# Performance work log

Measured on AMD Instinct MI355X. Metric: run time of the kernel, lower is better.

Reference implementation:

```python
import jax, jax.numpy as jnp
import numpy as np

B, N, D = 4, 4096, 128
LOSS_WEIGHT = 1.0  # module hardcodes self.loss_weight = 1.0


def setup_inputs() -> dict:
    key = jax.random.key(0)
    k1, k2 = jax.random.split(key)
    corr_pred = jax.random.normal(k1, (B, N, D), dtype=jnp.float32)
    corr_target = jax.random.normal(k2, (B, N, D), dtype=jnp.float32)
    return {"corr_pred": corr_pred, "corr_target": corr_target}


def chamfer_distance(x, y):
    # x: [B, N, D], y: [B, N, D]
    x2 = jnp.sum(x * x, axis=-1)                      # [B, N]  diag of x @ x^T
    y2 = jnp.sum(y * y, axis=-1)                      # [B, N]  diag of y @ y^T
    zz = jnp.einsum('bnd,bmd->bnm', x, y)             # [B, N, N]
    # P[b,i,j] = ||x_i||^2 + ||y_j||^2 - 2 x_i . y_j
    P = x2[:, :, None] + y2[:, None, :] - 2.0 * zz
    P = jnp.clip(P, 0.0, 100.0)
    return jnp.mean(jnp.min(P, axis=1)) + jnp.mean(jnp.min(P, axis=2))


def reference(corr_pred, corr_target):
    chamfer = chamfer_distance(corr_pred, corr_target)
    return LOSS_WEIGHT * chamfer / corr_target.shape[0]
```

## Files before the change

kernel.cpp:

```cpp
#include <hip/hip_runtime.h>
#include <hip/hip_bf16.h>

#define B_ 4
#define N_ 4096
#define D_ 128
#define EPB (N_ * D_)
#define COFF 1024.0f

typedef float f32x4 __attribute__((ext_vector_type(4)));
typedef int   int8v __attribute__((ext_vector_type(8)));
typedef int   int4v __attribute__((ext_vector_type(4)));

#define SQRT2 1.41421356237309515f


__global__ __launch_bounds__(256) void prep_kernel(
    const float* __restrict__ X, const float* __restrict__ Y,
    unsigned char* __restrict__ Xb, unsigned char* __restrict__ Yb,
    float* __restrict__ x2, float* __restrict__ y2,
    int* __restrict__ rowmin, int* __restrict__ colmin)
{
    const int which = blockIdx.y;
    const float* __restrict__ src = which ? Y : X;
    unsigned char* __restrict__ dst = which ? Yb : Xb;
    float* __restrict__ nrm = which ? y2 : x2;
    int* __restrict__ mn = which ? colmin : rowmin;

    const int t = threadIdx.x;
    const int r = t >> 4, c = t & 15;
    const int rgG = blockIdx.x;
    const int row = rgG * 16 + r;

    const float4 v0 = *(const float4*)(src + (size_t)row * D_ + c * 8);
    const float4 v1 = *(const float4*)(src + (size_t)row * D_ + c * 8 + 4);

    float sq = v0.x * v0.x;
    sq = fmaf(v0.y, v0.y, sq); sq = fmaf(v0.z, v0.z, sq); sq = fmaf(v0.w, v0.w, sq);
    sq = fmaf(v1.x, v1.x, sq); sq = fmaf(v1.y, v1.y, sq);
    sq = fmaf(v1.z, v1.z, sq); sq = fmaf(v1.w, v1.w, sq);
    #pragma unroll
    for (int m = 1; m < 16; m <<= 1) sq += __shfl_xor(sq, m);

    unsigned lo = 0, hi = 0;
    lo = __builtin_amdgcn_cvt_pk_fp8_f32(v0.x * SQRT2, v0.y * SQRT2, lo, false);
    lo = __builtin_amdgcn_cvt_pk_fp8_f32(v0.z * SQRT2, v0.w * SQRT2, lo, true);
    hi = __builtin_amdgcn_cvt_pk_fp8_f32(v1.x * SQRT2, v1.y * SQRT2, hi, false);
    hi = __builtin_amdgcn_cvt_pk_fp8_f32(v1.z * SQRT2, v1.w * SQRT2, hi, true);

    const int b = row >> 12;
    const int rg = (row & (N_ - 1)) >> 4;
    uint2 packed; packed.x = lo; packed.y = hi;
    *(uint2*)(dst + (size_t)b * EPB + rg * 2048 + (c >> 2) * 512
              + r * 32 + (c & 3) * 8) = packed;

    if (c == 0) {
        nrm[row] = sq;
        mn[row] = 0x7f7fffff;
    }
}


#define PREF(B0, B1, Y0, Y1, H) do {                                          \
    const int cb_ = jc * 256 + (H) * 32;                                      \
    const unsigned char* bp0_ = Yp + (size_t)(cb_ >> 4) * 2048                \
                               + quad * 512 + l16 * 32;                       \
    const int4v lo0_ = *(const int4v*)(bp0_);                                 \
    const int4v hi0_ = *(const int4v*)(bp0_ + 16);                            \
    const int4v lo1_ = *(const int4v*)(bp0_ + 2048);                          \
    const int4v hi1_ = *(const int4v*)(bp0_ + 2064);                          \
    B0 = (int8v){lo0_.x, lo0_.y, lo0_.z, lo0_.w, hi0_.x, hi0_.y, hi0_.z, hi0_.w}; \
    B1 = (int8v){lo1_.x, lo1_.y, lo1_.z, lo1_.w, hi1_.x, hi1_.y, hi1_.z, hi1_.w}; \
    Y0 = y2[(size_t)b * N_ + cb_ + l16];                                      \
    Y1 = y2[(size_t)b * N_ + cb_ + 16 + l16];                                 \
} while (0)

#define STEP(B0, B1, Y0, Y1, H) do {                                          \
    f32x4 acc0_[4], acc1_[4];                                                 \
    _Pragma("unroll")                                                         \
    for (int rt = 0; rt < 4; rt++) {                                          \
        acc0_[rt] = (f32x4){0.f, 0.f, 0.f, 0.f};                              \
        acc1_[rt] = (f32x4){0.f, 0.f, 0.f, 0.f};                              \
    }                                                                         \
    _Pragma("unroll")                                                         \
    for (int rt = 0; rt < 4; rt++) {                                          \
        acc0_[rt] = __builtin_amdgcn_mfma_scale_f32_16x16x128_f8f6f4(         \
            af[rt], B0, acc0_[rt], 0, 0, 0, 127, 0, 127);                     \
        acc1_[rt] = __builtin_amdgcn_mfma_scale_f32_16x16x128_f8f6f4(         \
            af[rt], B1, acc1_[rt], 0, 0, 0, 127, 0, 127);                     \
    }                                                                         \
    float cm0_ = 3.0e38f, cm1_ = 3.0e38f;                                     \
    _Pragma("unroll")                                                         \
    for (int rt = 0; rt < 4; rt++)                                            \
    _Pragma("unroll")                                                         \
    for (int i = 0; i < 4; i++) {                                             \
        const float xv_ = x2v[rt][i];                                         \
        const float a0_ = acc0_[rt][i], a1_ = acc1_[rt][i];                   \
        rmin[rt][i] = fminf(rmin[rt][i], fminf(Y0 - a0_, Y1 - a1_));          \
        cm0_ = fminf(cm0_, xv_ - a0_);                                        \
        cm1_ = fminf(cm1_, xv_ - a1_);                                        \
    }                                                                         \
    {                                                                         \
        const int cb_ = jc * 256 + (H) * 32;                                  \
        float v0_ = fminf(cm0_, __shfl_xor(cm0_, 16));                        \
        v0_ = fminf(v0_, __shfl_xor(v0_, 32));                                \
        float v1_ = fminf(cm1_, __shfl_xor(cm1_, 16));                        \
        v1_ = fminf(v1_, __shfl_xor(v1_, 32));                                \
        if (quad == 0) {                                                      \
            atomicMin(&colmin[(size_t)b * N_ + cb_ + l16],                    \
                      __float_as_int(v0_ + COFF));                            \
            atomicMin(&colmin[(size_t)b * N_ + cb_ + 16 + l16],               \
                      __float_as_int(v1_ + COFF));                            \
        }                                                                     \
    }                                                                         \
} while (0)

__global__ __launch_bounds__(256, 2) void chamfer_mfma(
    const unsigned char* __restrict__ Xb, const unsigned char* __restrict__ Yb,
    const float* __restrict__ x2, const float* __restrict__ y2,
    int* __restrict__ rowmin, int* __restrict__ colmin)
{
    const int b = blockIdx.z;
    const int iT = blockIdx.y;
    const int jc = blockIdx.x;
    const int tid = threadIdx.x;
    const int wave = tid >> 6, lane = tid & 63;
    const int quad = lane >> 4, l16 = lane & 15;
    const int rowBase = iT * 256 + wave * 64;

    const unsigned char* __restrict__ Xp = Xb + (size_t)b * EPB;
    const unsigned char* __restrict__ Yp = Yb + (size_t)b * EPB;

    int8v af[4];
    #pragma unroll
    for (int rt = 0; rt < 4; rt++) {
        const unsigned char* ap = Xp + ((rowBase >> 4) + rt) * 2048
                                 + quad * 512 + l16 * 32;
        const int4v lo = *(const int4v*)(ap);
        const int4v hi = *(const int4v*)(ap + 16);
        af[rt] = (int8v){lo.x, lo.y, lo.z, lo.w, hi.x, hi.y, hi.z, hi.w};
    }
    f32x4 x2v[4];
    #pragma unroll
    for (int rt = 0; rt < 4; rt++)
        x2v[rt] = *(const f32x4*)(x2 + (size_t)b * N_ + rowBase + rt * 16 + quad * 4);

    float rmin[4][4];
    #pragma unroll
    for (int rt = 0; rt < 4; rt++)
        #pragma unroll
        for (int i = 0; i < 4; i++) rmin[rt][i] = 3.0e38f;

    int8v bA0, bA1, bB0, bB1;
    float yA0, yA1, yB0, yB1;
    PREF(bA0, bA1, yA0, yA1, 0);

    #pragma clang loop unroll(disable)
    for (int sp = 0; sp < 4; ++sp) {
        const int h0 = sp * 2;
        PREF(bB0, bB1, yB0, yB1, h0 + 1);
        STEP(bA0, bA1, yA0, yA1, h0);
        if (sp < 3)
            PREF(bA0, bA1, yA0, yA1, h0 + 2);
        STEP(bB0, bB1, yB0, yB1, h0 + 1);
    }

    #pragma unroll
    for (int rt = 0; rt < 4; rt++)
        #pragma unroll
        for (int i = 0; i < 4; i++) {
            float v = rmin[rt][i];
            #pragma unroll
            for (int m = 1; m < 16; m <<= 1) v = fminf(v, __shfl_xor(v, m));
            if (l16 == 0) {
                float c = fminf(fmaxf(x2v[rt][i] + v, 0.0f), 100.0f);
                atomicMin(&rowmin[(size_t)b * N_ + rowBase + rt * 16 + quad * 4 + i],
                          __float_as_int(c));
            }
        }
}

__global__ __launch_bounds__(256) void finalize1_kernel(
    const int* __restrict__ rowmin, const int* __restrict__ colmin,
    const float* __restrict__ y2, float* __restrict__ partial)
{
    const int i = blockIdx.x * 256 + threadIdx.x;
    float s;
    {
        int4 v = ((const int4*)rowmin)[i];
        s  = __int_as_float(v.x) + __int_as_float(v.y) +
             __int_as_float(v.z) + __int_as_float(v.w);
        int4 c = ((const int4*)colmin)[i];
        float4 yv = ((const float4*)y2)[i];
        s += fminf(fmaxf(__int_as_float(c.x) - COFF + yv.x, 0.f), 100.f);
        s += fminf(fmaxf(__int_as_float(c.y) - COFF + yv.y, 0.f), 100.f);
        s += fminf(fmaxf(__int_as_float(c.z) - COFF + yv.z, 0.f), 100.f);
        s += fminf(fmaxf(__int_as_float(c.w) - COFF + yv.w, 0.f), 100.f);
    }
    #pragma unroll
    for (int m = 1; m < 64; m <<= 1) s += __shfl_xor(s, m);
    __shared__ float sm[4];
    if ((threadIdx.x & 63) == 0) sm[threadIdx.x >> 6] = s;
    __syncthreads();
    if (threadIdx.x == 0)
        partial[blockIdx.x] = sm[0] + sm[1] + sm[2] + sm[3];
}

__global__ __launch_bounds__(64) void finalize2_kernel(
    const float* __restrict__ partial, float* __restrict__ out)
{
    const int l = threadIdx.x;
    float s = (l < 16) ? partial[l] : 0.f;
    #pragma unroll
    for (int m = 1; m < 16; m <<= 1) s += __shfl_xor(s, m);
    if (l == 0)
        out[0] = s / ((float)B_ * (float)N_) / (float)B_;
}

extern "C" void kernel_launch(void* const* d_in, const int* in_sizes, int n_in,
                              void* d_out, int out_size, void* d_ws, size_t ws_size,
                              hipStream_t stream) {
    const float* X = (const float*)d_in[0];
    const float* Y = (const float*)d_in[1];

    char* ws = (char*)d_ws;
    const size_t f8_bytes = (size_t)B_ * N_ * D_;
    unsigned char* Xb = (unsigned char*)ws;
    unsigned char* Yb = (unsigned char*)(ws + f8_bytes);
    char* ws2 = ws + 2 * f8_bytes;
    const size_t vec_bytes = (size_t)B_ * N_ * 4;
    float* x2      = (float*)(ws2);
    float* y2      = (float*)(ws2 + vec_bytes);
    int*   rowmin  = (int*)  (ws2 + 2 * vec_bytes);
    int*   colmin  = (int*)  (ws2 + 3 * vec_bytes);
    float* partial = (float*)(ws2 + 4 * vec_bytes);
    float* out = (float*)d_out;

    prep_kernel<<<dim3(B_ * N_ / 16, 2), 256, 0, stream>>>(
        X, Y, Xb, Yb, x2, y2, rowmin, colmin);
    chamfer_mfma<<<dim3(16, N_ / 256, B_), 256, 0, stream>>>(
        Xb, Yb, x2, y2, rowmin, colmin);
    finalize1_kernel<<<16, 256, 0, stream>>>(rowmin, colmin, y2, partial);
    finalize2_kernel<<<1, 64, 0, stream>>>(partial, out);
}
```

Before: 91.38 us.

## Replace global atomicMin reductions with per-block partial buffers reduced in finalize

Row and column minima are no longer merged with global atomicMin. Instead, each block and wave writes its partial minima to dedicated slices of a workspace buffer, and finalize1 reduces over the 16 row partials and 64 column partials for each element. This removes atomic contention and the init stores in prep, at the cost of a much larger workspace (about 80 vectors) and more memory traffic in the finalize pass, which now runs on 64 blocks.

```diff
diff --git a/kernel.cpp b/kernel.cpp
--- a/kernel.cpp
+++ b/kernel.cpp
@@ -5,7 +5,6 @@
 #define N_ 4096
 #define D_ 128
 #define EPB (N_ * D_)
-#define COFF 1024.0f
 
 typedef float f32x4 __attribute__((ext_vector_type(4)));
 typedef int   int8v __attribute__((ext_vector_type(8)));
@@ -17,14 +16,12 @@
 __global__ __launch_bounds__(256) void prep_kernel(
     const float* __restrict__ X, const float* __restrict__ Y,
     unsigned char* __restrict__ Xb, unsigned char* __restrict__ Yb,
-    float* __restrict__ x2, float* __restrict__ y2,
-    int* __restrict__ rowmin, int* __restrict__ colmin)
+    float* __restrict__ x2, float* __restrict__ y2)
 {
     const int which = blockIdx.y;
     const float* __restrict__ src = which ? Y : X;
     unsigned char* __restrict__ dst = which ? Yb : Xb;
     float* __restrict__ nrm = which ? y2 : x2;
-    int* __restrict__ mn = which ? colmin : rowmin;
 
     const int t = threadIdx.x;
     const int r = t >> 4, c = t & 15;
@@ -53,10 +50,7 @@
     *(uint2*)(dst + (size_t)b * EPB + rg * 2048 + (c >> 2) * 512
               + r * 32 + (c & 3) * 8) = packed;
 
-    if (c == 0) {
-        nrm[row] = sq;
-        mn[row] = 0x7f7fffff;
-    }
+    if (c == 0) nrm[row] = sq;
 }
 
 
@@ -106,10 +100,8 @@
         float v1_ = fminf(cm1_, __shfl_xor(cm1_, 16));                        \
         v1_ = fminf(v1_, __shfl_xor(v1_, 32));                                \
         if (quad == 0) {                                                      \
-            atomicMin(&colmin[(size_t)b * N_ + cb_ + l16],                    \
-                      __float_as_int(v0_ + COFF));                            \
-            atomicMin(&colmin[(size_t)b * N_ + cb_ + 16 + l16],               \
-                      __float_as_int(v1_ + COFF));                            \
+            cpart[cpb + cb_ + l16] = v0_;                                     \
+            cpart[cpb + cb_ + 16 + l16] = v1_;                                \
         }                                                                     \
     }                                                                         \
 } while (0)
@@ -117,7 +109,7 @@
 __global__ __launch_bounds__(256, 2) void chamfer_mfma(
     const unsigned char* __restrict__ Xb, const unsigned char* __restrict__ Yb,
     const float* __restrict__ x2, const float* __restrict__ y2,
-    int* __restrict__ rowmin, int* __restrict__ colmin)
+    float* __restrict__ rpart, float* __restrict__ cpart)
 {
     const int b = blockIdx.z;
     const int iT = blockIdx.y;
@@ -126,6 +118,8 @@
     const int wave = tid >> 6, lane = tid & 63;
     const int quad = lane >> 4, l16 = lane & 15;
     const int rowBase = iT * 256 + wave * 64;
+    const size_t cpb = (size_t)((b * 16 + iT) * 4 + wave) * N_;
+    const size_t rpb = (size_t)(b * 16 + jc) * N_;
 
     const unsigned char* __restrict__ Xp = Xb + (size_t)b * EPB;
     const unsigned char* __restrict__ Yp = Yb + (size_t)b * EPB;
@@ -172,30 +166,31 @@
             #pragma unroll
             for (int m = 1; m < 16; m <<= 1) v = fminf(v, __shfl_xor(v, m));
             if (l16 == 0) {
-                float c = fminf(fmaxf(x2v[rt][i] + v, 0.0f), 100.0f);
-                atomicMin(&rowmin[(size_t)b * N_ + rowBase + rt * 16 + quad * 4 + i],
-                          __float_as_int(c));
+                rpart[rpb + rowBase + rt * 16 + quad * 4 + i] =
+                    fminf(fmaxf(x2v[rt][i] + v, 0.0f), 100.0f);
             }
         }
 }
 
 __global__ __launch_bounds__(256) void finalize1_kernel(
-    const int* __restrict__ rowmin, const int* __restrict__ colmin,
+    const float* __restrict__ rpart, const float* __restrict__ cpart,
     const float* __restrict__ y2, float* __restrict__ partial)
 {
-    const int i = blockIdx.x * 256 + threadIdx.x;
-    float s;
-    {
-        int4 v = ((const int4*)rowmin)[i];
-        s  = __int_as_float(v.x) + __int_as_float(v.y) +
-             __int_as_float(v.z) + __int_as_float(v.w);
-        int4 c = ((const int4*)colmin)[i];
-        float4 yv = ((const float4*)y2)[i];
-        s += fminf(fmaxf(__int_as_float(c.x) - COFF + yv.x, 0.f), 100.f);
-        s += fminf(fmaxf(__int_as_float(c.y) - COFF + yv.y, 0.f), 100.f);
-        s += fminf(fmaxf(__int_as_float(c.z) - COFF + yv.z, 0.f), 100.f);
-        s += fminf(fmaxf(__int_as_float(c.w) - COFF + yv.w, 0.f), 100.f);
-    }
+    const int e = blockIdx.x * 256 + threadIdx.x;
+    const int b = e >> 12, i = e & (N_ - 1);
+
+    float rm = 3.0e38f;
+    #pragma unroll
+    for (int j = 0; j < 16; j++)
+        rm = fminf(rm, rpart[(size_t)(b * 16 + j) * N_ + i]);
+
+    float cm = 3.0e38f;
+    #pragma unroll
+    for (int p = 0; p < 64; p++)
+        cm = fminf(cm, cpart[(size_t)(b * 64 + p) * N_ + i]);
+
+    float s = rm + fminf(fmaxf(cm + y2[e], 0.0f), 100.0f);
+
     #pragma unroll
     for (int m = 1; m < 64; m <<= 1) s += __shfl_xor(s, m);
     __shared__ float sm[4];
@@ -209,9 +204,9 @@
     const float* __restrict__ partial, float* __restrict__ out)
 {
     const int l = threadIdx.x;
-    float s = (l < 16) ? partial[l] : 0.f;
-    #pragma unroll
-    for (int m = 1; m < 16; m <<= 1) s += __shfl_xor(s, m);
+    float s = partial[l];
+    #pragma unroll
+    for (int m = 1; m < 64; m <<= 1) s += __shfl_xor(s, m);
     if (l == 0)
         out[0] = s / ((float)B_ * (float)N_) / (float)B_;
 }
@@ -230,15 +225,15 @@
     const size_t vec_bytes = (size_t)B_ * N_ * 4;
     float* x2      = (float*)(ws2);
     float* y2      = (float*)(ws2 + vec_bytes);
-    int*   rowmin  = (int*)  (ws2 + 2 * vec_bytes);
-    int*   colmin  = (int*)  (ws2 + 3 * vec_bytes);
-    float* partial = (float*)(ws2 + 4 * vec_bytes);
+    float* rpart   = (float*)(ws2 + 2 * vec_bytes);
+    float* cpart   = (float*)(ws2 + 2 * vec_bytes + 16 * vec_bytes);
+    float* partial = (float*)(ws2 + 2 * vec_bytes + 80 * vec_bytes);
     float* out = (float*)d_out;
 
     prep_kernel<<<dim3(B_ * N_ / 16, 2), 256, 0, stream>>>(
-        X, Y, Xb, Yb, x2, y2, rowmin, colmin);
+        X, Y, Xb, Yb, x2, y2);
     chamfer_mfma<<<dim3(16, N_ / 256, B_), 256, 0, stream>>>(
-        Xb, Yb, x2, y2, rowmin, colmin);
-    finalize1_kernel<<<16, 256, 0, stream>>>(rowmin, colmin, y2, partial);
+        Xb, Yb, x2, y2, rpart, cpart);
+    finalize1_kernel<<<64, 256, 0, stream>>>(rpart, cpart, y2, partial);
     finalize2_kernel<<<1, 64, 0, stream>>>(partial, out);
 }
```

Result: no change. 90.81 us (-0.6%).
